# Optimization experiments

Measured on AMD Instinct MI355X. Metric: run time of the kernel, lower is better.

Reference implementation:

```python
import jax, jax.numpy as jnp
import numpy as np

N_NODES = 20000
N_EDGES = 320000
NFEAT = 128
NHID = 64
NCLASS = 16
HEADS = 4
NLAYERS = 3
DT = 1.0
EPS = 1e-5
NEG_SLOPE = 0.2
# softplus(1.0) for Ks, omega, zeta (raw values all 1.0, non-learnable)
SP1 = float(np.log1p(np.exp(1.0)))


def rms_norm(x):
    rms = jnp.sqrt(jnp.mean(x * x, axis=-1, keepdims=True) + EPS)
    return x / rms


def gat_conv(x, src, dst, W_gat, att_src, att_dst, b_gat):
    # x: [N, NHID] -> per-head projections h: [N, H, NHID]
    h = (x @ W_gat).reshape(N_NODES, HEADS, NHID)
    a_src = jnp.sum(h * att_src[None], axis=-1)  # [N, H]
    a_dst = jnp.sum(h * att_dst[None], axis=-1)  # [N, H]
    e = jax.nn.leaky_relu(a_src[src] + a_dst[dst], NEG_SLOPE)  # [E, H]
    # segment softmax over incoming edges of each destination node
    e_max = jax.ops.segment_max(e, dst, num_segments=N_NODES)
    e_max = jnp.where(jnp.isfinite(e_max), e_max, 0.0)
    ex = jnp.exp(e - e_max[dst])
    denom = jax.ops.segment_sum(ex, dst, num_segments=N_NODES)
    alpha = ex / (denom[dst] + 1e-16)  # [E, H]
    msg = h[src] * alpha[:, :, None]  # [E, H, NHID]
    out = jax.ops.segment_sum(msg, dst, num_segments=N_NODES)  # [N, H, NHID]
    return out.reshape(N_NODES, HEADS * NHID) + b_gat


def setup_inputs() -> dict:
    key = jax.random.key(0)
    ks = jax.random.split(key, 10)
    s = 0.05
    x = jax.random.normal(ks[0], (N_NODES, NFEAT), dtype=jnp.float32)
    edge_index = jax.random.randint(ks[1], (2, N_EDGES), 0, N_NODES, dtype=jnp.int64)
    return {
        "x": x,
        "edge_index": edge_index,
        "W_enc": jax.random.normal(ks[2], (NFEAT, NHID), dtype=jnp.float32) * s,
        "b_enc": jnp.zeros((NHID,), dtype=jnp.float32),
        "W_gat": jax.random.normal(ks[3], (NHID, HEADS * NHID), dtype=jnp.float32) * s,
        "att_src": jax.random.normal(ks[4], (HEADS, NHID), dtype=jnp.float32) * s,
        "att_dst": jax.random.normal(ks[5], (HEADS, NHID), dtype=jnp.float32) * s,
        "b_gat": jnp.zeros((HEADS * NHID,), dtype=jnp.float32),
        "W_dec": jax.random.normal(ks[6], (NHID, NCLASS), dtype=jnp.float32) * s,
        "b_dec": jnp.zeros((NCLASS,), dtype=jnp.float32),
    }


def reference(x, edge_index, W_enc, b_enc, W_gat, att_src, att_dst, b_gat, W_dec, b_dec):
    # eval mode: dropout is identity
    Ks, omega, zeta = SP1, SP1, SP1
    omega_sq = omega * omega
    # PyG GATConv add_self_loops=True
    loops = jnp.arange(N_NODES, dtype=edge_index.dtype)
    src = jnp.concatenate([edge_index[0], loops])
    dst = jnp.concatenate([edge_index[1], loops])

    Y = jax.nn.relu(x @ W_enc + b_enc)
    X = Y
    for _ in range(NLAYERS):
        conv = jax.nn.elu(gat_conv(X, src, dst, W_gat, att_src, att_dst, b_gat))
        # faithful to original: view(N, -1, heads).mean(-1) on [N, heads*nhid]
        agg = conv.reshape(N_NODES, NHID, HEADS).mean(axis=-1)
        Y = Y + DT * (Ks * agg - 2.0 * zeta * omega * Y - omega_sq * X)
        X = X + DT * Y
        X = rms_norm(X)
        Y = rms_norm(Y)
    return X @ W_dec + b_dec
```

## Files before the change

kernel.cpp:

```cpp
#include <hip/hip_runtime.h>
#include <hip/hip_bf16.h>

#define DEV static __device__ __forceinline__

constexpr int N_NODES = 20000;
constexpr int N_EDGES = 320000;
constexpr int NFEAT = 128;
constexpr int NHID = 64;
constexpr int NCLASS = 16;
constexpr int HEADS = 4;
constexpr int HD = HEADS * NHID;
constexpr float EPSV = 1e-5f;
constexpr float SLOPE = 0.2f;
constexpr float SP1 = 1.3132616875182228f;

typedef __attribute__((ext_vector_type(8))) short short8;
typedef __attribute__((ext_vector_type(4))) float float4v;

DEV float bf2f(__hip_bfloat16 v) { return __bfloat162float(v); }
DEV float bfbits2f(unsigned short b) { return __uint_as_float(((unsigned)b) << 16); }
DEV short f2bfbits(float v) { return (short)__bfloat16_as_ushort(__float2bfloat16(v)); }
DEV float lrelu(float v) { return v > 0.f ? v : SLOPE * v; }
DEV int clampn(int v) { return min(max(v, 0), N_NODES - 1); }

DEV float ldf(const void* p, int i, int f32) {
  return f32 ? ((const float*)p)[i] : bf2f(((const __hip_bfloat16*)p)[i]);
}
DEV int eload(const int* e32, int is64, int idx) {
  if (is64) return (int)(((const long long*)e32)[idx]);
  return e32[idx];
}

DEV float wsum(float v) {
#pragma unroll
  for (int m = 32; m > 0; m >>= 1) v += __shfl_xor(v, m, 64);
  return v;
}
DEV float qsum(float v) {
#pragma unroll
  for (int m = 1; m < 16; m <<= 1) v += __shfl_xor(v, m, 64);
  return v;
}
DEV float hsel(float4 v, int hd) {
  return (hd == 0) ? v.x : (hd == 1) ? v.y : (hd == 2) ? v.z : v.w;
}
DEV void acc8_i8(float* acc, int lo, int hi, float a) {
  acc[0] = fmaf((float)(signed char)(lo), a, acc[0]);
  acc[1] = fmaf((float)(signed char)(lo >> 8), a, acc[1]);
  acc[2] = fmaf((float)(signed char)(lo >> 16), a, acc[2]);
  acc[3] = fmaf((float)(lo >> 24), a, acc[3]);
  acc[4] = fmaf((float)(signed char)(hi), a, acc[4]);
  acc[5] = fmaf((float)(signed char)(hi >> 8), a, acc[5]);
  acc[6] = fmaf((float)(signed char)(hi >> 16), a, acc[6]);
  acc[7] = fmaf((float)(hi >> 24), a, acc[7]);
}

__global__ __launch_bounds__(256) void k_detect_pack(const int* __restrict__ edge,
                                                     const unsigned* __restrict__ xw,
                                                     const void* __restrict__ W_enc,
                                                     const void* __restrict__ W_gat,
                                                     int* __restrict__ flag,
                                                     short* __restrict__ packE,
                                                     short* __restrict__ packG) {
  __shared__ int sflag[2];
  int tid = threadIdx.x;
  if (tid < 64) {
    int v = edge[2 * tid + 1];
    unsigned long long nz = __ballot(v != 0);
    int bad = 0;
#pragma unroll
    for (int j = 0; j < 4; ++j) {
      unsigned w = xw[tid * 4 + j];
      unsigned ex = ((w & 0xFFFFu) >> 7) & 0xFFu;
      if (ex >= 0x90u) bad = 1;
    }
    unsigned long long anybad = __ballot(bad != 0);
    if (tid == 0) {
      sflag[0] = (nz == 0ULL) ? 1 : 0;
      sflag[1] = (anybad != 0ULL) ? 1 : 0;
      flag[0] = sflag[0];
      flag[1] = sflag[1];
    }
  }
  __syncthreads();
  int f32 = sflag[1];
  int wv = tid >> 6, lane = tid & 63;
  int quad = lane >> 4, m16 = lane & 15;
#pragma unroll
  for (int ks = 0; ks < 4; ++ks)
#pragma unroll
    for (int j = 0; j < 8; ++j)
      packE[(ks * 256 + tid) * 8 + j] =
          f2bfbits(ldf(W_enc, (ks * 32 + quad * 8 + j) * NHID + wv * 16 + m16, f32));
#pragma unroll
  for (int t = 0; t < 4; ++t)
#pragma unroll
    for (int ks = 0; ks < 2; ++ks)
#pragma unroll
      for (int j = 0; j < 8; ++j)
        packG[((t * 2 + ks) * 256 + tid) * 8 + j] =
            f2bfbits(ldf(W_gat, (ks * 32 + quad * 8 + j) * HD + wv * 64 + t * 16 + m16, f32));
}

__global__ void k_hist(const int* __restrict__ edge, const int* __restrict__ flag,
                       int* __restrict__ counts) {
  int e = blockIdx.x * blockDim.x + threadIdx.x;
  if (e < N_EDGES) {
    int d = clampn(eload(edge, flag[0], N_EDGES + e));
    atomicAdd(&counts[d], 1);
  }
}

__global__ __launch_bounds__(1024) void k_scan(const int* __restrict__ counts,
                                               int* __restrict__ rowptr,
                                               int* __restrict__ cursor) {
  __shared__ int part[1024];
  int t = threadIdx.x;
  const int CH = (N_NODES + 1023) / 1024;
  int b = t * CH, e = min(b + CH, N_NODES);
  int s = 0;
  for (int i = b; i < e; ++i) s += counts[i];
  part[t] = s;
  __syncthreads();
  for (int off = 1; off < 1024; off <<= 1) {
    int v = (t >= off) ? part[t - off] : 0;
    __syncthreads();
    part[t] += v;
    __syncthreads();
  }
  int run = (t == 0) ? 0 : part[t - 1];
  for (int i = b; i < e; ++i) {
    rowptr[i] = run;
    cursor[i] = run;
    run += counts[i];
  }
  if (t == 1023) rowptr[N_NODES] = N_EDGES;
}

__global__ void k_scatter(const int* __restrict__ edge, const int* __restrict__ flag,
                          int* __restrict__ cursor, int* __restrict__ ssort) {
  int e = blockIdx.x * blockDim.x + threadIdx.x;
  if (e < N_EDGES) {
    int is64 = flag[0];
    int s = clampn(eload(edge, is64, e));
    int d = clampn(eload(edge, is64, N_EDGES + e));
    int pos = atomicAdd(&cursor[d], 1);
    if (pos >= 0 && pos < N_EDGES) ssort[pos] = s;
  }
}

__global__ __launch_bounds__(256) void k_encoder(const void* __restrict__ x,
                                                 const short* __restrict__ packE,
                                                 const void* __restrict__ b_enc,
                                                 const int* __restrict__ flag,
                                                 float* __restrict__ X, float* __restrict__ Y) {
  int f32 = flag[1];
  int tid = threadIdx.x;
  int wv = tid >> 6, lane = tid & 63;
  int quad = lane >> 4, m16 = lane & 15;
  int n0 = blockIdx.x * 16;
  int c0 = wv * 16;

  float4v acc = {0.f, 0.f, 0.f, 0.f};
#pragma unroll
  for (int ks = 0; ks < 4; ++ks) {
    short8 bfrag = *(const short8*)(packE + (ks * 256 + tid) * 8);
    short8 afrag;
    size_t xoff = (size_t)(n0 + m16) * NFEAT + ks * 32 + quad * 8;
    if (f32) {
      float4 f0 = *(const float4*)((const float*)x + xoff);
      float4 f1 = *(const float4*)((const float*)x + xoff + 4);
      afrag[0] = f2bfbits(f0.x); afrag[1] = f2bfbits(f0.y);
      afrag[2] = f2bfbits(f0.z); afrag[3] = f2bfbits(f0.w);
      afrag[4] = f2bfbits(f1.x); afrag[5] = f2bfbits(f1.y);
      afrag[6] = f2bfbits(f1.z); afrag[7] = f2bfbits(f1.w);
    } else {
      afrag = *(const short8*)((const short*)x + xoff);
    }
    acc = __builtin_amdgcn_mfma_f32_16x16x32_bf16(afrag, bfrag, acc, 0, 0, 0);
  }

  float bias = ldf(b_enc, c0 + m16, f32);
#pragma unroll
  for (int r = 0; r < 4; ++r) {
    int n = n0 + quad * 4 + r;
    float yv = fmaxf(acc[r] + bias, 0.f);
    size_t idx = (size_t)n * NHID + c0 + m16;
    X[idx] = yv;
    Y[idx] = yv;
  }
}

__global__ __launch_bounds__(256) void k_proj(const float* __restrict__ X,
                                              const short* __restrict__ packG,
                                              const void* __restrict__ att_src,
                                              const void* __restrict__ att_dst,
                                              const int* __restrict__ flag,
                                              signed char* __restrict__ hb,
                                              float* __restrict__ hscale,
                                              float* __restrict__ a_src,
                                              float* __restrict__ a_dst) {
  __shared__ float smax[4][16];
  int f32 = flag[1];
  int tid = threadIdx.x;
  int wv = tid >> 6, lane = tid & 63;
  int quad = lane >> 4, m16 = lane & 15;
  int n0 = blockIdx.x * 16;

  short8 afrag[2];
#pragma unroll
  for (int ks = 0; ks < 2; ++ks) {
    size_t xoff = (size_t)(n0 + m16) * NHID + ks * 32 + quad * 8;
    float4 f0 = *(const float4*)(X + xoff);
    float4 f1 = *(const float4*)(X + xoff + 4);
    afrag[ks][0] = f2bfbits(f0.x); afrag[ks][1] = f2bfbits(f0.y);
    afrag[ks][2] = f2bfbits(f0.z); afrag[ks][3] = f2bfbits(f0.w);
    afrag[ks][4] = f2bfbits(f1.x); afrag[ks][5] = f2bfbits(f1.y);
    afrag[ks][6] = f2bfbits(f1.z); afrag[ks][7] = f2bfbits(f1.w);
  }

  float4v acc[4];
#pragma unroll
  for (int t = 0; t < 4; ++t) {
    acc[t] = (float4v){0.f, 0.f, 0.f, 0.f};
#pragma unroll
    for (int ks = 0; ks < 2; ++ks) {
      short8 bfrag = *(const short8*)(packG + ((t * 2 + ks) * 256 + tid) * 8);
      acc[t] = __builtin_amdgcn_mfma_f32_16x16x32_bf16(afrag[ks], bfrag, acc[t], 0, 0, 0);
    }
  }

  float amax[4];
#pragma unroll
  for (int r = 0; r < 4; ++r) {
    float m = fmaxf(fmaxf(fabsf(acc[0][r]), fabsf(acc[1][r])),
                    fmaxf(fabsf(acc[2][r]), fabsf(acc[3][r])));
#pragma unroll
    for (int sh = 1; sh < 16; sh <<= 1) m = fmaxf(m, __shfl_xor(m, sh, 64));
    amax[r] = m;
  }
  if (m16 == 0) {
#pragma unroll
    for (int r = 0; r < 4; ++r) smax[wv][quad * 4 + r] = amax[r];
  }
  __syncthreads();
  float inv[4];
#pragma unroll
  for (int r = 0; r < 4; ++r) {
    int row = quad * 4 + r;
    float m = fmaxf(fmaxf(smax[0][row], smax[1][row]), fmaxf(smax[2][row], smax[3][row]));
    inv[r] = (m > 0.f) ? 127.f / m : 0.f;
  }
  if (tid < 16) {
    float m = fmaxf(fmaxf(smax[0][tid], smax[1][tid]), fmaxf(smax[2][tid], smax[3][tid]));
    hscale[n0 + tid] = m * (1.f / 127.f);
  }

  float avs[4], avd[4];
#pragma unroll
  for (int t = 0; t < 4; ++t) {
    avs[t] = ldf(att_src, wv * 64 + t * 16 + m16, f32);
    avd[t] = ldf(att_dst, wv * 64 + t * 16 + m16, f32);
  }
  float ps[4], pd[4];
#pragma unroll
  for (int r = 0; r < 4; ++r) { ps[r] = 0.f; pd[r] = 0.f; }
#pragma unroll
  for (int t = 0; t < 4; ++t) {
#pragma unroll
    for (int r = 0; r < 4; ++r) {
      int n = n0 + quad * 4 + r;
      hb[(size_t)n * HD + wv * 64 + t * 16 + m16] =
          (signed char)__float2int_rn(acc[t][r] * inv[r]);
      ps[r] = fmaf(acc[t][r], avs[t], ps[r]);
      pd[r] = fmaf(acc[t][r], avd[t], pd[r]);
    }
  }
#pragma unroll
  for (int r = 0; r < 4; ++r) {
    float s = qsum(ps[r]);
    float dq = qsum(pd[r]);
    if (m16 == 0) {
      int n = n0 + quad * 4 + r;
      a_src[n * HEADS + wv] = s;
      a_dst[n * HEADS + wv] = dq;
    }
  }
}

__global__ __launch_bounds__(256) void k_layer(const signed char* __restrict__ hb,
                                               const float* __restrict__ hscale,
                                               const float* __restrict__ a_src,
                                               const float* __restrict__ a_dst,
                                               const int* __restrict__ rowptr,
                                               const int* __restrict__ srcs,
                                               float* __restrict__ we,
                                               const void* __restrict__ b_gat,
                                               const int* __restrict__ flag,
                                               float* __restrict__ X, float* __restrict__ Y) {
  int wave = threadIdx.x >> 6, lane = threadIdx.x & 63;
  int half = lane >> 5, l32 = lane & 31, head = l32 >> 3;
  int f32 = flag[1];
  int d = blockIdx.x * 4 + wave;
  if (d >= N_NODES) return;
  int beg = rowptr[d];
  int end = rowptr[d + 1];
  beg = min(max(beg, 0), N_EDGES);
  end = min(max(end, beg), N_EDGES);
  int deg = end - beg;
  const float4 adv = *(const float4*)(a_dst + d * 4);

  float sm0 = 0.f, sm1 = 0.f, sm2 = 0.f, sm3 = 0.f;
  for (int i = lane; i < deg; i += 64) {
    int p = beg + i;
    int s = clampn(srcs[p]);
    const float4 ar = *(const float4*)(a_src + s * 4);
    float scl = hscale[s];
    float w0 = __expf(lrelu(ar.x + adv.x));
    float w1 = __expf(lrelu(ar.y + adv.y));
    float w2 = __expf(lrelu(ar.z + adv.z));
    float w3 = __expf(lrelu(ar.w + adv.w));
    *(float4*)(we + (size_t)p * 4) = make_float4(w0 * scl, w1 * scl, w2 * scl, w3 * scl);
    sm0 += w0; sm1 += w1; sm2 += w2; sm3 += w3;
  }
  sm0 = wsum(sm0); sm1 = wsum(sm1); sm2 = wsum(sm2); sm3 = wsum(sm3);
  const float4 ars = *(const float4*)(a_src + d * 4);
  float4 wself = make_float4(__expf(lrelu(ars.x + adv.x)), __expf(lrelu(ars.y + adv.y)),
                             __expf(lrelu(ars.z + adv.z)), __expf(lrelu(ars.w + adv.w)));
  sm0 += wself.x; sm1 += wself.y; sm2 += wself.z; sm3 += wself.w;

  float invh = 1.f / (hsel(make_float4(sm0, sm1, sm2, sm3), head) + 1e-16f);

  float acc[8];
#pragma unroll
  for (int k = 0; k < 8; ++k) acc[k] = 0.f;
  {
    float a = (half == 0) ? hsel(wself, head) * hscale[d] : 0.f;
    uint2 hv = *(const uint2*)(hb + (size_t)d * HD + l32 * 8);
    acc8_i8(acc, (int)hv.x, (int)hv.y, a);
  }
  int p = beg;
  for (; p + 8 <= end; p += 8) {
    int q0 = p + half, q1 = p + 2 + half, q2 = p + 4 + half, q3 = p + 6 + half;
    int s0 = clampn(srcs[q0]), s1 = clampn(srcs[q1]);
    int s2 = clampn(srcs[q2]), s3 = clampn(srcs[q3]);
    float a0 = we[(size_t)q0 * 4 + head];
    float a1 = we[(size_t)q1 * 4 + head];
    float a2 = we[(size_t)q2 * 4 + head];
    float a3 = we[(size_t)q3 * 4 + head];
    uint2 h0 = *(const uint2*)(hb + (size_t)s0 * HD + l32 * 8);
    uint2 h1 = *(const uint2*)(hb + (size_t)s1 * HD + l32 * 8);
    uint2 h2 = *(const uint2*)(hb + (size_t)s2 * HD + l32 * 8);
    uint2 h3 = *(const uint2*)(hb + (size_t)s3 * HD + l32 * 8);
    acc8_i8(acc, (int)h0.x, (int)h0.y, a0);
    acc8_i8(acc, (int)h1.x, (int)h1.y, a1);
    acc8_i8(acc, (int)h2.x, (int)h2.y, a2);
    acc8_i8(acc, (int)h3.x, (int)h3.y, a3);
  }
  for (; p < end; p += 2) {
    int q = p + half;
    bool act = q < end;
    int s = clampn(srcs[act ? q : end - 1]);
    float a = act ? we[(size_t)q * 4 + head] : 0.f;
    uint2 hv = *(const uint2*)(hb + (size_t)s * HD + l32 * 8);
    acc8_i8(acc, (int)hv.x, (int)hv.y, a);
  }
#pragma unroll
  for (int k = 0; k < 8; ++k) acc[k] += __shfl_xor(acc[k], 32, 64);

  float cg[8];
#pragma unroll
  for (int k = 0; k < 8; ++k) {
    float c = acc[k] * invh + ldf(b_gat, l32 * 8 + k, f32);
    cg[k] = c > 0.f ? c : expm1f(c);
  }
  float agg0 = 0.25f * (cg[0] + cg[1] + cg[2] + cg[3]);
  float agg1 = 0.25f * (cg[4] + cg[5] + cg[6] + cg[7]);

  size_t ix = (size_t)d * NHID + l32 * 2;
  float xv0 = X[ix], xv1 = X[ix + 1];
  float yv0 = Y[ix], yv1 = Y[ix + 1];
  float yn0 = yv0 + (SP1 * agg0 - 2.f * SP1 * SP1 * yv0 - SP1 * SP1 * xv0);
  float yn1 = yv1 + (SP1 * agg1 - 2.f * SP1 * SP1 * yv1 - SP1 * SP1 * xv1);
  float xn0 = xv0 + yn0;
  float xn1 = xv1 + yn1;

  float msx = wsum(xn0 * xn0 + xn1 * xn1) * (1.f / 128.f);
  float rx = rsqrtf(msx + EPSV);
  float msy = wsum(yn0 * yn0 + yn1 * yn1) * (1.f / 128.f);
  float ry = rsqrtf(msy + EPSV);
  X[ix] = xn0 * rx; X[ix + 1] = xn1 * rx;
  Y[ix] = yn0 * ry; Y[ix + 1] = yn1 * ry;
}

__global__ __launch_bounds__(256) void k_dec(const float* __restrict__ X,
                                             const void* __restrict__ W_dec,
                                             const void* __restrict__ b_dec,
                                             const int* __restrict__ flag,
                                             float* __restrict__ out) {
  __shared__ float Wl[NHID * NCLASS];
  __shared__ float bl[NCLASS];
  int f32 = flag[1];
  int tid = threadIdx.x;
  for (int i = tid; i < NHID * NCLASS; i += 256) Wl[i] = ldf(W_dec, i, f32);
  if (tid < NCLASS) bl[tid] = ldf(b_dec, tid, f32);
  __syncthreads();
  int g = blockIdx.x * 256 + tid;
  if (g >= N_NODES * NCLASS) return;
  int n = g >> 4, c = g & 15;
  const float* xr = X + (size_t)n * NHID;
  float acc = bl[c];
#pragma unroll
  for (int k = 0; k < NHID; ++k) acc = fmaf(xr[k], Wl[k * NCLASS + c], acc);
  if (!(acc == acc) || fabsf(acc) > 1e6f) acc = 777.0f;
  out[g] = acc;
}

extern "C" void kernel_launch(void* const* d_in, const int* in_sizes, int n_in,
                              void* d_out, int out_size, void* d_ws, size_t ws_size,
                              hipStream_t stream) {
  const void* x       = d_in[0];
  const int*  edge    = (const int*)d_in[1];
  const void* W_enc   = d_in[2];
  const void* b_enc   = d_in[3];
  const void* W_gat   = d_in[4];
  const void* att_src = d_in[5];
  const void* att_dst = d_in[6];
  const void* b_gat   = d_in[7];
  const void* W_dec   = d_in[8];
  const void* b_dec   = d_in[9];

  char* ws = (char*)d_ws;
  size_t off = 0;
  auto alloc = [&](size_t bytes) -> void* {
    if (off + bytes > ws_size) off = 0;
    void* p = ws + off;
    off = (off + bytes + 255) & ~(size_t)255;
    return p;
  };
  int*   flag   = (int*)alloc(256);
  int*   counts = (int*)alloc((size_t)N_NODES * 4);
  int*   rowptr = (int*)alloc((size_t)(N_NODES + 1) * 4);
  int*   cursor = (int*)alloc((size_t)N_NODES * 4);
  int*   ssort  = (int*)alloc((size_t)N_EDGES * 4);
  float* a_src  = (float*)alloc((size_t)N_NODES * HEADS * 4);
  float* a_dst  = (float*)alloc((size_t)N_NODES * HEADS * 4);
  float* X      = (float*)alloc((size_t)N_NODES * NHID * 4);
  float* Y      = (float*)alloc((size_t)N_NODES * NHID * 4);
  float* hscale = (float*)alloc((size_t)N_NODES * 4);
  short* packE  = (short*)alloc((size_t)4 * 256 * 8 * 2);
  short* packG  = (short*)alloc((size_t)8 * 256 * 8 * 2);
  signed char* hb = (signed char*)alloc((size_t)N_NODES * HD);
  float* we     = (float*)alloc((size_t)N_EDGES * HEADS * 4);

  hipMemsetAsync(counts, 0, (size_t)N_NODES * 4, stream);
  k_detect_pack<<<1, 256, 0, stream>>>(edge, (const unsigned*)x, W_enc, W_gat, flag, packE, packG);
  k_hist<<<(N_EDGES + 255) / 256, 256, 0, stream>>>(edge, flag, counts);
  k_scan<<<1, 1024, 0, stream>>>(counts, rowptr, cursor);
  k_scatter<<<(N_EDGES + 255) / 256, 256, 0, stream>>>(edge, flag, cursor, ssort);

  k_encoder<<<N_NODES / 16, 256, 0, stream>>>(x, packE, b_enc, flag, X, Y);
  for (int l = 0; l < 3; ++l) {
    k_proj<<<N_NODES / 16, 256, 0, stream>>>(X, packG, att_src, att_dst, flag, hb, hscale, a_src, a_dst);
    k_layer<<<N_NODES / 4, 256, 0, stream>>>(hb, hscale, a_src, a_dst, rowptr, ssort, we, b_gat, flag, X, Y);
  }
  k_dec<<<(N_NODES * NCLASS + 255) / 256, 256, 0, stream>>>(X, W_dec, b_dec, flag, (float*)d_out);
}
```

Baseline: 344.4 us.

## Fuse edge softmax weights into aggregation loop and interleave node scale with a_src

Removes the separate per-destination pass that computed exp attention weights into a global per-edge buffer and summed them. Each lane now computes the exponentiated weight inline while gathering neighbor features, accumulating the softmax denominator alongside. a_src and the per-node int8 scale are packed into one interleaved nodeinfo array, so one float2 load per edge supplies both. This drops the per-edge write and reread of the weights buffer at the cost of redundant exp calls across lanes, and it also drops the max-free exponent reuse pattern.

Result: faster. 334.0 us (-3.0%).

```diff
diff --git a/kernel.cpp b/kernel.cpp
--- a/kernel.cpp
+++ b/kernel.cpp
@@ -18,7 +18,6 @@
 typedef __attribute__((ext_vector_type(4))) float float4v;
 
 DEV float bf2f(__hip_bfloat16 v) { return __bfloat162float(v); }
-DEV float bfbits2f(unsigned short b) { return __uint_as_float(((unsigned)b) << 16); }
 DEV short f2bfbits(float v) { return (short)__bfloat16_as_ushort(__float2bfloat16(v)); }
 DEV float lrelu(float v) { return v > 0.f ? v : SLOPE * v; }
 DEV int clampn(int v) { return min(max(v, 0), N_NODES - 1); }
@@ -40,9 +39,6 @@
 #pragma unroll
   for (int m = 1; m < 16; m <<= 1) v += __shfl_xor(v, m, 64);
   return v;
-}
-DEV float hsel(float4 v, int hd) {
-  return (hd == 0) ? v.x : (hd == 1) ? v.y : (hd == 2) ? v.z : v.w;
 }
 DEV void acc8_i8(float* acc, int lo, int hi, float a) {
   acc[0] = fmaf((float)(signed char)(lo), a, acc[0]);
@@ -197,8 +193,7 @@
                                               const void* __restrict__ att_dst,
                                               const int* __restrict__ flag,
                                               signed char* __restrict__ hb,
-                                              float* __restrict__ hscale,
-                                              float* __restrict__ a_src,
+                                              float* __restrict__ nodeinfo,
                                               float* __restrict__ a_dst) {
   __shared__ float smax[4][16];
   int f32 = flag[1];
@@ -244,16 +239,13 @@
     for (int r = 0; r < 4; ++r) smax[wv][quad * 4 + r] = amax[r];
   }
   __syncthreads();
-  float inv[4];
+  float inv[4], rmax[4];
 #pragma unroll
   for (int r = 0; r < 4; ++r) {
     int row = quad * 4 + r;
     float m = fmaxf(fmaxf(smax[0][row], smax[1][row]), fmaxf(smax[2][row], smax[3][row]));
+    rmax[r] = m;
     inv[r] = (m > 0.f) ? 127.f / m : 0.f;
-  }
-  if (tid < 16) {
-    float m = fmaxf(fmaxf(smax[0][tid], smax[1][tid]), fmaxf(smax[2][tid], smax[3][tid]));
-    hscale[n0 + tid] = m * (1.f / 127.f);
   }
 
   float avs[4], avd[4];
@@ -282,19 +274,18 @@
     float dq = qsum(pd[r]);
     if (m16 == 0) {
       int n = n0 + quad * 4 + r;
-      a_src[n * HEADS + wv] = s;
+      nodeinfo[(size_t)n * 8 + wv * 2] = s;
+      nodeinfo[(size_t)n * 8 + wv * 2 + 1] = rmax[r] * (1.f / 127.f);
       a_dst[n * HEADS + wv] = dq;
     }
   }
 }
 
 __global__ __launch_bounds__(256) void k_layer(const signed char* __restrict__ hb,
-                                               const float* __restrict__ hscale,
-                                               const float* __restrict__ a_src,
+                                               const float* __restrict__ nodeinfo,
                                                const float* __restrict__ a_dst,
                                                const int* __restrict__ rowptr,
                                                const int* __restrict__ srcs,
-                                               float* __restrict__ we,
                                                const void* __restrict__ b_gat,
                                                const int* __restrict__ flag,
                                                float* __restrict__ X, float* __restrict__ Y) {
@@ -307,66 +298,59 @@
   int end = rowptr[d + 1];
   beg = min(max(beg, 0), N_EDGES);
   end = min(max(end, beg), N_EDGES);
-  int deg = end - beg;
-  const float4 adv = *(const float4*)(a_dst + d * 4);
-
-  float sm0 = 0.f, sm1 = 0.f, sm2 = 0.f, sm3 = 0.f;
-  for (int i = lane; i < deg; i += 64) {
-    int p = beg + i;
-    int s = clampn(srcs[p]);
-    const float4 ar = *(const float4*)(a_src + s * 4);
-    float scl = hscale[s];
-    float w0 = __expf(lrelu(ar.x + adv.x));
-    float w1 = __expf(lrelu(ar.y + adv.y));
-    float w2 = __expf(lrelu(ar.z + adv.z));
-    float w3 = __expf(lrelu(ar.w + adv.w));
-    *(float4*)(we + (size_t)p * 4) = make_float4(w0 * scl, w1 * scl, w2 * scl, w3 * scl);
-    sm0 += w0; sm1 += w1; sm2 += w2; sm3 += w3;
-  }
-  sm0 = wsum(sm0); sm1 = wsum(sm1); sm2 = wsum(sm2); sm3 = wsum(sm3);
-  const float4 ars = *(const float4*)(a_src + d * 4);
-  float4 wself = make_float4(__expf(lrelu(ars.x + adv.x)), __expf(lrelu(ars.y + adv.y)),
-                             __expf(lrelu(ars.z + adv.z)), __expf(lrelu(ars.w + adv.w)));
-  sm0 += wself.x; sm1 += wself.y; sm2 += wself.z; sm3 += wself.w;
-
-  float invh = 1.f / (hsel(make_float4(sm0, sm1, sm2, sm3), head) + 1e-16f);
+  float advh = a_dst[d * 4 + head];
 
   float acc[8];
 #pragma unroll
   for (int k = 0; k < 8; ++k) acc[k] = 0.f;
+  float sw = 0.f;
+
   {
-    float a = (half == 0) ? hsel(wself, head) * hscale[d] : 0.f;
-    uint2 hv = *(const uint2*)(hb + (size_t)d * HD + l32 * 8);
-    acc8_i8(acc, (int)hv.x, (int)hv.y, a);
+    float2 nid = *(const float2*)(nodeinfo + (size_t)d * 8 + head * 2);
+    float wself = __expf(lrelu(nid.x + advh));
+    if (half == 0) {
+      sw = wself;
+      uint2 hv = *(const uint2*)(hb + (size_t)d * HD + l32 * 8);
+      acc8_i8(acc, (int)hv.x, (int)hv.y, wself * nid.y);
+    }
   }
   int p = beg;
   for (; p + 8 <= end; p += 8) {
     int q0 = p + half, q1 = p + 2 + half, q2 = p + 4 + half, q3 = p + 6 + half;
     int s0 = clampn(srcs[q0]), s1 = clampn(srcs[q1]);
     int s2 = clampn(srcs[q2]), s3 = clampn(srcs[q3]);
-    float a0 = we[(size_t)q0 * 4 + head];
-    float a1 = we[(size_t)q1 * 4 + head];
-    float a2 = we[(size_t)q2 * 4 + head];
-    float a3 = we[(size_t)q3 * 4 + head];
+    float2 n0v = *(const float2*)(nodeinfo + (size_t)s0 * 8 + head * 2);
+    float2 n1v = *(const float2*)(nodeinfo + (size_t)s1 * 8 + head * 2);
+    float2 n2v = *(const float2*)(nodeinfo + (size_t)s2 * 8 + head * 2);
+    float2 n3v = *(const float2*)(nodeinfo + (size_t)s3 * 8 + head * 2);
     uint2 h0 = *(const uint2*)(hb + (size_t)s0 * HD + l32 * 8);
     uint2 h1 = *(const uint2*)(hb + (size_t)s1 * HD + l32 * 8);
     uint2 h2 = *(const uint2*)(hb + (size_t)s2 * HD + l32 * 8);
     uint2 h3 = *(const uint2*)(hb + (size_t)s3 * HD + l32 * 8);
-    acc8_i8(acc, (int)h0.x, (int)h0.y, a0);
-    acc8_i8(acc, (int)h1.x, (int)h1.y, a1);
-    acc8_i8(acc, (int)h2.x, (int)h2.y, a2);
-    acc8_i8(acc, (int)h3.x, (int)h3.y, a3);
+    float w0 = __expf(lrelu(n0v.x + advh));
+    float w1 = __expf(lrelu(n1v.x + advh));
+    float w2 = __expf(lrelu(n2v.x + advh));
+    float w3 = __expf(lrelu(n3v.x + advh));
+    sw += w0 + w1 + w2 + w3;
+    acc8_i8(acc, (int)h0.x, (int)h0.y, w0 * n0v.y);
+    acc8_i8(acc, (int)h1.x, (int)h1.y, w1 * n1v.y);
+    acc8_i8(acc, (int)h2.x, (int)h2.y, w2 * n2v.y);
+    acc8_i8(acc, (int)h3.x, (int)h3.y, w3 * n3v.y);
   }
   for (; p < end; p += 2) {
     int q = p + half;
     bool act = q < end;
     int s = clampn(srcs[act ? q : end - 1]);
-    float a = act ? we[(size_t)q * 4 + head] : 0.f;
+    float2 nv = *(const float2*)(nodeinfo + (size_t)s * 8 + head * 2);
     uint2 hv = *(const uint2*)(hb + (size_t)s * HD + l32 * 8);
-    acc8_i8(acc, (int)hv.x, (int)hv.y, a);
-  }
+    float w = act ? __expf(lrelu(nv.x + advh)) : 0.f;
+    sw += w;
+    acc8_i8(acc, (int)hv.x, (int)hv.y, w * nv.y);
+  }
+  sw += __shfl_xor(sw, 32, 64);
 #pragma unroll
   for (int k = 0; k < 8; ++k) acc[k] += __shfl_xor(acc[k], 32, 64);
+  float invh = 1.f / (sw + 1e-16f);
 
   float cg[8];
 #pragma unroll
@@ -438,20 +422,18 @@
     off = (off + bytes + 255) & ~(size_t)255;
     return p;
   };
-  int*   flag   = (int*)alloc(256);
-  int*   counts = (int*)alloc((size_t)N_NODES * 4);
-  int*   rowptr = (int*)alloc((size_t)(N_NODES + 1) * 4);
-  int*   cursor = (int*)alloc((size_t)N_NODES * 4);
-  int*   ssort  = (int*)alloc((size_t)N_EDGES * 4);
-  float* a_src  = (float*)alloc((size_t)N_NODES * HEADS * 4);
-  float* a_dst  = (float*)alloc((size_t)N_NODES * HEADS * 4);
-  float* X      = (float*)alloc((size_t)N_NODES * NHID * 4);
-  float* Y      = (float*)alloc((size_t)N_NODES * NHID * 4);
-  float* hscale = (float*)alloc((size_t)N_NODES * 4);
-  short* packE  = (short*)alloc((size_t)4 * 256 * 8 * 2);
-  short* packG  = (short*)alloc((size_t)8 * 256 * 8 * 2);
+  int*   flag    = (int*)alloc(256);
+  int*   counts  = (int*)alloc((size_t)N_NODES * 4);
+  int*   rowptr  = (int*)alloc((size_t)(N_NODES + 1) * 4);
+  int*   cursor  = (int*)alloc((size_t)N_NODES * 4);
+  int*   ssort   = (int*)alloc((size_t)N_EDGES * 4);
+  float* nodeinfo= (float*)alloc((size_t)N_NODES * 8 * 4);
+  float* a_dst   = (float*)alloc((size_t)N_NODES * HEADS * 4);
+  float* X       = (float*)alloc((size_t)N_NODES * NHID * 4);
+  float* Y       = (float*)alloc((size_t)N_NODES * NHID * 4);
+  short* packE   = (short*)alloc((size_t)4 * 256 * 8 * 2);
+  short* packG   = (short*)alloc((size_t)8 * 256 * 8 * 2);
   signed char* hb = (signed char*)alloc((size_t)N_NODES * HD);
-  float* we     = (float*)alloc((size_t)N_EDGES * HEADS * 4);
 
   hipMemsetAsync(counts, 0, (size_t)N_NODES * 4, stream);
   k_detect_pack<<<1, 256, 0, stream>>>(edge, (const unsigned*)x, W_enc, W_gat, flag, packE, packG);
@@ -461,8 +443,8 @@
 
   k_encoder<<<N_NODES / 16, 256, 0, stream>>>(x, packE, b_enc, flag, X, Y);
   for (int l = 0; l < 3; ++l) {
-    k_proj<<<N_NODES / 16, 256, 0, stream>>>(X, packG, att_src, att_dst, flag, hb, hscale, a_src, a_dst);
-    k_layer<<<N_NODES / 4, 256, 0, stream>>>(hb, hscale, a_src, a_dst, rowptr, ssort, we, b_gat, flag, X, Y);
+    k_proj<<<N_NODES / 16, 256, 0, stream>>>(X, packG, att_src, att_dst, flag, hb, nodeinfo, a_dst);
+    k_layer<<<N_NODES / 4, 256, 0, stream>>>(hb, nodeinfo, a_dst, rowptr, ssort, b_gat, flag, X, Y);
   }
   k_dec<<<(N_NODES * NCLASS + 255) / 256, 256, 0, stream>>>(X, W_dec, b_dec, flag, (float*)d_out);
 }
```
